# Kernel tuning notes

Measured on AMD Instinct MI355X. Metric: run time of the kernel, lower is better.

## Reference

```python
import jax, jax.numpy as jnp
import numpy as np

N_NODES = 100000
N_EDGES = 1200000
NUM_GRAPHS = 128
IN_DIM = 5
HIDDEN = 64


def setup_inputs() -> dict:
    key = jax.random.key(0)
    ks = jax.random.split(key, 12)
    x = jax.random.normal(ks[0], (N_NODES, IN_DIM), dtype=jnp.float32)
    edge_index = jax.random.randint(ks[1], (2, N_EDGES), 0, N_NODES, dtype=jnp.int64 if jax.config.read('jax_enable_x64') else jnp.int32)
    batch = jnp.sort(jax.random.randint(ks[2], (N_NODES,), 0, NUM_GRAPHS, dtype=jnp.int32))
    s = lambda fan_in: 1.0 / np.sqrt(fan_in)
    return {
        'x': x,
        'edge_index': edge_index,
        'batch': batch,
        'w_rel1': jax.random.normal(ks[3], (IN_DIM, HIDDEN), dtype=jnp.float32) * s(IN_DIM),
        'b_rel1': jnp.zeros((HIDDEN,), dtype=jnp.float32),
        'w_root1': jax.random.normal(ks[4], (IN_DIM, HIDDEN), dtype=jnp.float32) * s(IN_DIM),
        'w_rel2': jax.random.normal(ks[5], (HIDDEN, HIDDEN), dtype=jnp.float32) * s(HIDDEN),
        'b_rel2': jnp.zeros((HIDDEN,), dtype=jnp.float32),
        'w_root2': jax.random.normal(ks[6], (HIDDEN, HIDDEN), dtype=jnp.float32) * s(HIDDEN),
        'w_h1': jax.random.normal(ks[7], (2 * HIDDEN, HIDDEN), dtype=jnp.float32) * s(2 * HIDDEN),
        'b_h1': jnp.zeros((HIDDEN,), dtype=jnp.float32),
        'w_h2': jax.random.normal(ks[8], (HIDDEN, 1), dtype=jnp.float32) * s(HIDDEN),
        'b_h2': jnp.zeros((1,), dtype=jnp.float32),
    }


def _graph_conv(x, src, dst, w_rel, b_rel, w_root):
    # PyG GraphConv (aggr='add'): out = aggr(x_src -> dst) @ W_rel + b_rel + x @ W_root
    agg = jax.ops.segment_sum(x[src], dst, num_segments=N_NODES)
    return agg @ w_rel + b_rel + x @ w_root


def reference(x, edge_index, batch,
              w_rel1, b_rel1, w_root1,
              w_rel2, b_rel2, w_root2,
              w_h1, b_h1, w_h2, b_h2):
    src, dst = edge_index[0], edge_index[1]
    h = jax.nn.relu(_graph_conv(x, src, dst, w_rel1, b_rel1, w_root1))
    h = jax.nn.relu(_graph_conv(h, src, dst, w_rel2, b_rel2, w_root2))
    # global add + mean pooling over graphs
    add_pool = jax.ops.segment_sum(h, batch, num_segments=NUM_GRAPHS)
    counts = jax.ops.segment_sum(jnp.ones((N_NODES,), h.dtype), batch, num_segments=NUM_GRAPHS)
    mean_pool = add_pool / jnp.maximum(counts, 1.0)[:, None]
    g = jnp.concatenate([mean_pool, add_pool], axis=1)  # [G, 2*HIDDEN]
    out = jax.nn.relu(g @ w_h1 + b_h1) @ w_h2 + b_h2
    return out.squeeze(-1)
```

## Files before the change

kernel.cpp:

```cpp
#include <hip/hip_runtime.h>
#include <hip/hip_bf16.h>

#define N_NODES    100000
#define N_EDGES    1200000
#define NUM_GRAPHS 128
#define IN_DIM     5
#define HIDDEN     64
#define M_TILES    (N_NODES / 16)
#define NI4        (N_EDGES / 4)

#define CB    391
#define CBLK  256
#define EPB   ((NI4 + CBLK - 1) / CBLK)

typedef __attribute__((ext_vector_type(8))) short short8;
typedef __attribute__((ext_vector_type(4))) float f32x4;

__device__ __forceinline__ unsigned short f2bs(float f) {
    union { float f; unsigned u; } v; v.f = f;
    return (unsigned short)((v.u + 0x7FFFu + ((v.u >> 16) & 1u)) >> 16);
}
__device__ __forceinline__ float bs2f(unsigned short s) {
    union { unsigned u; float f; } v; v.u = ((unsigned)s) << 16;
    return v.f;
}
__device__ __forceinline__ float blo(unsigned p) { return bs2f((unsigned short)(p & 0xffff)); }
__device__ __forceinline__ float bhi(unsigned p) { return bs2f((unsigned short)(p >> 16)); }
__device__ __forceinline__ unsigned pack2(float a, float b) {
    return ((unsigned)f2bs(b) << 16) | (unsigned)f2bs(a);
}

__device__ __forceinline__ unsigned char f2f8(float f) {
    union { float f; unsigned u; } v; v.f = f * 0x1p-120f;
    unsigned u = v.u + 0x7FFFFu + ((v.u >> 20) & 1u);
    return (unsigned char)(u >> 20);
}
__device__ __forceinline__ float f82f(unsigned b) {
    union { unsigned u; float f; } v; v.u = (b & 0x7Fu) << 20;
    return v.f * 0x1p120f;
}


__global__ void coarse_count(const int* __restrict__ dst, int* __restrict__ gcnt,
                             const float* __restrict__ x, uint4* __restrict__ xb) {
    __shared__ int h[CB];
    int t = threadIdx.x, b = blockIdx.x;
    for (int i = t; i < CB; i += 256) h[i] = 0;
    __syncthreads();
    int i0 = b * EPB, i1 = min(i0 + EPB, NI4);
    for (int i = i0 + t; i < i1; i += 256) {
        int4 d = ((const int4*)dst)[i];
        atomicAdd(&h[d.x >> 8], 1);
        atomicAdd(&h[d.y >> 8], 1);
        atomicAdd(&h[d.z >> 8], 1);
        atomicAdd(&h[d.w >> 8], 1);
    }
    __syncthreads();
    for (int i = t; i < CB; i += 256) gcnt[b * CB + i] = h[i];

    for (int n = b * 256 + t; n < N_NODES; n += CBLK * 256) {
        const float* xr = x + (size_t)n * IN_DIM;
        uint4 o;
        o.x = pack2(xr[0], xr[1]);
        o.y = pack2(xr[2], xr[3]);
        o.z = pack2(xr[4], 0.0f);
        o.w = 0u;
        xb[n] = o;
    }
}

__global__ void block_scan(int* __restrict__ gcnt, int* __restrict__ btot) {
    __shared__ int s[CBLK];
    int k = blockIdx.x, t = threadIdx.x;
    int v = gcnt[t * CB + k];
    s[t] = v;
    __syncthreads();
    for (int off = 1; off < CBLK; off <<= 1) {
        int u = (t >= off) ? s[t - off] : 0;
        __syncthreads();
        s[t] += u;
        __syncthreads();
    }
    gcnt[t * CB + k] = s[t] - v;
    if (t == CBLK - 1) btot[k] = s[t];
}

__global__ void bucket_scan(const int* __restrict__ btot, int* __restrict__ bstart,
                            float* __restrict__ add_pool, int* __restrict__ ptr) {
    __shared__ int s[512];
    int t = threadIdx.x;
    int v = (t < CB) ? btot[t] : 0;
    s[t] = v;
    __syncthreads();
    for (int off = 1; off < 512; off <<= 1) {
        int u = (t >= off) ? s[t - off] : 0;
        __syncthreads();
        s[t] += u;
        __syncthreads();
    }
    if (t < CB) bstart[t] = s[t] - v;
    if (t == 0) { bstart[CB] = N_EDGES; ptr[N_NODES] = N_EDGES; }
    for (int i = t; i < NUM_GRAPHS * HIDDEN; i += 512) add_pool[i] = 0.0f;
}

__global__ void partition_k(const int* __restrict__ src, const int* __restrict__ dst,
                            const int* __restrict__ gcnt, const int* __restrict__ bstart,
                            int* __restrict__ part) {
    __shared__ int base[CB];
    __shared__ int h[CB];
    int t = threadIdx.x, b = blockIdx.x;
    for (int i = t; i < CB; i += 256) {
        base[i] = bstart[i] + gcnt[b * CB + i];
        h[i] = 0;
    }
    __syncthreads();
    int i0 = b * EPB, i1 = min(i0 + EPB, NI4);
    for (int i = i0 + t; i < i1; i += 256) {
        int4 s4 = ((const int4*)src)[i];
        int4 d4 = ((const int4*)dst)[i];
        int k, r;
        k = d4.x >> 8; r = atomicAdd(&h[k], 1); part[base[k] + r] = s4.x | ((d4.x & 255) << 17);
        k = d4.y >> 8; r = atomicAdd(&h[k], 1); part[base[k] + r] = s4.y | ((d4.y & 255) << 17);
        k = d4.z >> 8; r = atomicAdd(&h[k], 1); part[base[k] + r] = s4.z | ((d4.z & 255) << 17);
        k = d4.w >> 8; r = atomicAdd(&h[k], 1); part[base[k] + r] = s4.w | ((d4.w & 255) << 17);
    }
}

__global__ void fine_sort(const int* __restrict__ part, const int* __restrict__ bstart,
                          int* __restrict__ ptr, int* __restrict__ esrc) {
    __shared__ int fh[256];
    __shared__ int fo[256];
    __shared__ int fr[256];
    int k = blockIdx.x, t = threadIdx.x;
    int e0 = bstart[k], e1 = bstart[k + 1];
    fh[t] = 0; fr[t] = 0;
    __syncthreads();
    for (int e = e0 + t; e < e1; e += 256)
        atomicAdd(&fh[(part[e] >> 17) & 255], 1);
    __syncthreads();
    int v = fh[t];
    fo[t] = v;
    __syncthreads();
    for (int off = 1; off < 256; off <<= 1) {
        int u = (t >= off) ? fo[t - off] : 0;
        __syncthreads();
        fo[t] += u;
        __syncthreads();
    }
    int excl = fo[t] - v;
    int n = (k << 8) + t;
    if (n < N_NODES) ptr[n] = e0 + excl;
    fh[t] = excl;
    __syncthreads();
    for (int e = e0 + t; e < e1; e += 256) {
        int p = part[e];
        int d = (p >> 17) & 255;
        int r = atomicAdd(&fr[d], 1);
        esrc[e0 + fh[d] + r] = p & 0x1FFFF;
    }
}


__global__ void gather_mlp1(const uint4* __restrict__ xb,
                            const float* __restrict__ x,
                            const int* __restrict__ ptr,
                            const int* __restrict__ esrc,
                            const float* __restrict__ w_rel1,
                            const float* __restrict__ b_rel1,
                            const float* __restrict__ w_root1,
                            unsigned short* __restrict__ h1,
                            unsigned char* __restrict__ h1f8) {
    int t    = threadIdx.x;
    int ql   = t & 15;
    int grp  = (blockIdx.x * blockDim.x + t) >> 4;
    int ngrp = (gridDim.x * blockDim.x) >> 4;

    float wr[IN_DIM][4], wo[IN_DIM][4], bias[4];
#pragma unroll
    for (int j = 0; j < 4; ++j) {
        int ch = ql * 4 + j;
        bias[j] = b_rel1[ch];
#pragma unroll
        for (int k = 0; k < IN_DIM; ++k) {
            wr[k][j] = w_rel1[k * HIDDEN + ch];
            wo[k][j] = w_root1[k * HIDDEN + ch];
        }
    }

    for (int n = grp; n < N_NODES; n += ngrp) {
        int start = ptr[n], end = ptr[n + 1];
        float a[IN_DIM] = {0.f, 0.f, 0.f, 0.f, 0.f};
        for (int e = start + ql; e < end; e += 16) {
            uint4 p = xb[esrc[e]];
            a[0] += blo(p.x); a[1] += bhi(p.x);
            a[2] += blo(p.y); a[3] += bhi(p.y);
            a[4] += blo(p.z);
        }
#pragma unroll
        for (int k = 0; k < IN_DIM; ++k) {
            a[k] += __shfl_xor(a[k], 1, 64);
            a[k] += __shfl_xor(a[k], 2, 64);
            a[k] += __shfl_xor(a[k], 4, 64);
            a[k] += __shfl_xor(a[k], 8, 64);
        }
        float xr[IN_DIM];
#pragma unroll
        for (int k = 0; k < IN_DIM; ++k) xr[k] = x[(size_t)n * IN_DIM + k];

        unsigned short hv[4];
        unsigned char  hf[4];
#pragma unroll
        for (int j = 0; j < 4; ++j) {
            float acc = bias[j];
#pragma unroll
            for (int k = 0; k < IN_DIM; ++k)
                acc += a[k] * wr[k][j] + xr[k] * wo[k][j];
            float h = fmaxf(acc, 0.0f);
            hv[j] = f2bs(h);
            hf[j] = f2f8(h);
        }
        ushort4 v4; v4.x = hv[0]; v4.y = hv[1]; v4.z = hv[2]; v4.w = hv[3];
        *(ushort4*)(h1 + (size_t)n * HIDDEN + ql * 4) = v4;
        uchar4 c4; c4.x = hf[0]; c4.y = hf[1]; c4.z = hf[2]; c4.w = hf[3];
        *(uchar4*)(h1f8 + (size_t)n * HIDDEN + ql * 4) = c4;
    }
}

__global__ void gather2_fp8(const unsigned* __restrict__ rows,
                            const int* __restrict__ ptr,
                            const int* __restrict__ esrc,
                            uint2* __restrict__ agg2) {
    int t    = threadIdx.x;
    int ql   = t & 15;
    int grp  = (blockIdx.x * blockDim.x + t) >> 4;
    int ngrp = (gridDim.x * blockDim.x) >> 4;

    for (int n = grp; n < N_NODES; n += ngrp) {
        int start = ptr[n], end = ptr[n + 1];
        float4 a = {0.f, 0.f, 0.f, 0.f};
        float4 b = {0.f, 0.f, 0.f, 0.f};
        int e = start;
        for (; e + 1 < end; e += 2) {
            int s0 = esrc[e], s1 = esrc[e + 1];
            unsigned r0 = rows[(size_t)s0 * 16 + ql];
            unsigned r1 = rows[(size_t)s1 * 16 + ql];
            a.x += f82f(r0); a.y += f82f(r0 >> 8); a.z += f82f(r0 >> 16); a.w += f82f(r0 >> 24);
            b.x += f82f(r1); b.y += f82f(r1 >> 8); b.z += f82f(r1 >> 16); b.w += f82f(r1 >> 24);
        }
        if (e < end) {
            unsigned r0 = rows[(size_t)esrc[e] * 16 + ql];
            a.x += f82f(r0); a.y += f82f(r0 >> 8); a.z += f82f(r0 >> 16); a.w += f82f(r0 >> 24);
        }
        a.x += b.x; a.y += b.y; a.z += b.z; a.w += b.w;
        uint2 o;
        o.x = pack2(a.x, a.y);
        o.y = pack2(a.z, a.w);
        agg2[(size_t)n * 16 + ql] = o;
    }
}

__global__ void mlp2_pool(const unsigned short* __restrict__ agg2,
                          const unsigned short* __restrict__ h1,
                          const float* __restrict__ w_rel2,
                          const float* __restrict__ b_rel2,
                          const float* __restrict__ w_root2,
                          const int* __restrict__ batch,
                          float* __restrict__ add_pool) {
    int lane = threadIdx.x & 63;
    int wv   = threadIdx.x >> 6;
    int row  = lane & 15;
    int quad = lane >> 4;
    int n    = wv * 16 + row;

    short8 bwr[2], bwo[2];
#pragma unroll
    for (int s = 0; s < 2; ++s)
#pragma unroll
        for (int j = 0; j < 8; ++j) {
            int k = 32 * s + quad * 8 + j;
            bwr[s][j] = (short)f2bs(w_rel2[k * HIDDEN + n]);
            bwo[s][j] = (short)f2bs(w_root2[k * HIDDEN + n]);
        }
    float bias = b_rel2[n];

    for (int t = blockIdx.x; t < M_TILES; t += gridDim.x) {
        int m0 = t * 16;
        size_t rbase = (size_t)(m0 + row) * HIDDEN;
        short8 aa0 = *(const short8*)(agg2 + rbase + quad * 8);
        short8 aa1 = *(const short8*)(agg2 + rbase + 32 + quad * 8);
        short8 ah0 = *(const short8*)(h1   + rbase + quad * 8);
        short8 ah1 = *(const short8*)(h1   + rbase + 32 + quad * 8);

        f32x4 acc = {bias, bias, bias, bias};
        acc = __builtin_amdgcn_mfma_f32_16x16x32_bf16(aa0, bwr[0], acc, 0, 0, 0);
        acc = __builtin_amdgcn_mfma_f32_16x16x32_bf16(aa1, bwr[1], acc, 0, 0, 0);
        acc = __builtin_amdgcn_mfma_f32_16x16x32_bf16(ah0, bwo[0], acc, 0, 0, 0);
        acc = __builtin_amdgcn_mfma_f32_16x16x32_bf16(ah1, bwo[1], acc, 0, 0, 0);

        float hv0 = fmaxf(acc[0], 0.0f), hv1 = fmaxf(acc[1], 0.0f);
        float hv2 = fmaxf(acc[2], 0.0f), hv3 = fmaxf(acc[3], 0.0f);

        int gLo = batch[m0], gHi = batch[m0 + 15];
        if (gLo == gHi) {
            float s = (hv0 + hv1) + (hv2 + hv3);
            s += __shfl_xor(s, 16, 64);
            s += __shfl_xor(s, 32, 64);
            if (quad == 0)
                atomicAdd(&add_pool[gLo * HIDDEN + n], s);
        } else {
            int m = m0 + quad * 4;
            atomicAdd(&add_pool[batch[m]     * HIDDEN + n], hv0);
            atomicAdd(&add_pool[batch[m + 1] * HIDDEN + n], hv1);
            atomicAdd(&add_pool[batch[m + 2] * HIDDEN + n], hv2);
            atomicAdd(&add_pool[batch[m + 3] * HIDDEN + n], hv3);
        }
    }
}

__device__ __forceinline__ int lower_bound_i(const int* a, int n, int v) {
    int lo = 0, hi = n;
    while (lo < hi) { int mid = (lo + hi) >> 1; if (a[mid] < v) lo = mid + 1; else hi = mid; }
    return lo;
}

__global__ void head_mlp(const float* __restrict__ add_pool,
                         const int* __restrict__ batch,
                         const float* __restrict__ w_h1,
                         const float* __restrict__ b_h1,
                         const float* __restrict__ w_h2,
                         const float* __restrict__ b_h2,
                         float* __restrict__ out) {
    int g = blockIdx.x, t = threadIdx.x;

    __shared__ int s_cnt;
    if (t == 0) {
        int start = lower_bound_i(batch, N_NODES, g);
        int end   = lower_bound_i(batch, N_NODES, g + 1);
        s_cnt = end - start;
    }
    __syncthreads();
    float cnt = fmaxf((float)s_cnt, 1.0f);

    __shared__ float sg[2 * HIDDEN];
    float add = add_pool[(size_t)g * HIDDEN + t];
    sg[t]          = add / cnt;
    sg[HIDDEN + t] = add;
    __syncthreads();

    float hid = b_h1[t];
#pragma unroll 16
    for (int i = 0; i < 2 * HIDDEN; ++i)
        hid += sg[i] * w_h1[i * HIDDEN + t];
    hid = fmaxf(hid, 0.0f);

    float res = hid * w_h2[t];
    for (int off = 32; off > 0; off >>= 1)
        res += __shfl_down(res, off, 64);
    if (t == 0) out[g] = res + b_h2[0];
}

extern "C" void kernel_launch(void* const* d_in, const int* in_sizes, int n_in,
                              void* d_out, int out_size, void* d_ws, size_t ws_size,
                              hipStream_t stream) {
    const float* x       = (const float*)d_in[0];
    const int*   ei      = (const int*)d_in[1];
    const int*   src     = ei;
    const int*   dst     = ei + N_EDGES;
    const int*   batch   = (const int*)d_in[2];
    const float* w_rel1  = (const float*)d_in[3];
    const float* b_rel1  = (const float*)d_in[4];
    const float* w_root1 = (const float*)d_in[5];
    const float* w_rel2  = (const float*)d_in[6];
    const float* b_rel2  = (const float*)d_in[7];
    const float* w_root2 = (const float*)d_in[8];
    const float* w_h1    = (const float*)d_in[9];
    const float* b_h1    = (const float*)d_in[10];
    const float* w_h2    = (const float*)d_in[11];
    const float* b_h2    = (const float*)d_in[12];
    float* out = (float*)d_out;

    int* base = (int*)d_ws;
    int*   gcnt     = base;
    int*   btot     = gcnt + ((CBLK * CB + 3) & ~3);
    int*   bstart   = btot + ((CB + 3) & ~3);
    float* add_pool = (float*)(bstart + ((CB + 1 + 3) & ~3));
    int*   ptr      = (int*)(add_pool + NUM_GRAPHS * HIDDEN);
    int*   part     = ptr + ((N_NODES + 1 + 3) & ~3);
    int*   esrc     = part + N_EDGES;
    unsigned short* h1   = (unsigned short*)(esrc + N_EDGES);
    unsigned short* agg2 = h1 + (size_t)N_NODES * HIDDEN;
    unsigned char*  h1f8 = (unsigned char*)(agg2 + (size_t)N_NODES * HIDDEN);
    uint4*          xb   = (uint4*)(h1f8 + (size_t)N_NODES * HIDDEN);

    coarse_count<<<CBLK, 256, 0, stream>>>(dst, gcnt, x, xb);
    block_scan<<<CB, CBLK, 0, stream>>>(gcnt, btot);
    bucket_scan<<<1, 512, 0, stream>>>(btot, bstart, add_pool, ptr);
    partition_k<<<CBLK, 256, 0, stream>>>(src, dst, gcnt, bstart, part);
    fine_sort<<<CB, 256, 0, stream>>>(part, bstart, ptr, esrc);

    gather_mlp1<<<2048, 256, 0, stream>>>(xb, x, ptr, esrc, w_rel1, b_rel1, w_root1, h1, h1f8);
    gather2_fp8<<<2048, 256, 0, stream>>>((const unsigned*)h1f8, ptr, esrc, (uint2*)agg2);
    mlp2_pool<<<2048, 256, 0, stream>>>(agg2, h1, w_rel2, b_rel2, w_root2, batch, add_pool);
    head_mlp<<<NUM_GRAPHS, 64, 0, stream>>>(add_pool, batch, w_h1, b_h1, w_h2, b_h2, out);
}
```

Measured before the change: 191.2 us.

## Fuse fine sort with first-layer gather and unroll fp8 gather by four

The per-bucket fine sort kernel now goes on to compute layer-1 aggregation and the MLP for its 256 nodes, using the shared-memory offsets instead of re-reading ptr. This removes a kernel launch and lets the esrc entries just written be reused from cache. The cost is that the 391 blocks of this stage now carry the gather work, with less parallelism than the separate 2048-block launch. Separately, the second-layer fp8 gather is unrolled to four independent accumulators to raise memory-level parallelism.

New measurement: 195.4 us. 1.02x slower.

```diff
diff --git a/kernel.cpp b/kernel.cpp
--- a/kernel.cpp
+++ b/kernel.cpp
@@ -126,8 +126,15 @@
     }
 }
 
-__global__ void fine_sort(const int* __restrict__ part, const int* __restrict__ bstart,
-                          int* __restrict__ ptr, int* __restrict__ esrc) {
+__global__ void fine_gather1(const int* __restrict__ part, const int* __restrict__ bstart,
+                             int* __restrict__ ptr, int* __restrict__ esrc,
+                             const uint4* __restrict__ xb,
+                             const float* __restrict__ x,
+                             const float* __restrict__ w_rel1,
+                             const float* __restrict__ b_rel1,
+                             const float* __restrict__ w_root1,
+                             unsigned short* __restrict__ h1,
+                             unsigned char* __restrict__ h1f8) {
     __shared__ int fh[256];
     __shared__ int fo[256];
     __shared__ int fr[256];
@@ -148,8 +155,8 @@
         __syncthreads();
     }
     int excl = fo[t] - v;
-    int n = (k << 8) + t;
-    if (n < N_NODES) ptr[n] = e0 + excl;
+    int n_t = (k << 8) + t;
+    if (n_t < N_NODES) ptr[n_t] = e0 + excl;
     fh[t] = excl;
     __syncthreads();
     for (int e = e0 + t; e < e1; e += 256) {
@@ -158,37 +165,27 @@
         int r = atomicAdd(&fr[d], 1);
         esrc[e0 + fh[d] + r] = p & 0x1FFFF;
     }
-}
-
-
-__global__ void gather_mlp1(const uint4* __restrict__ xb,
-                            const float* __restrict__ x,
-                            const int* __restrict__ ptr,
-                            const int* __restrict__ esrc,
-                            const float* __restrict__ w_rel1,
-                            const float* __restrict__ b_rel1,
-                            const float* __restrict__ w_root1,
-                            unsigned short* __restrict__ h1,
-                            unsigned char* __restrict__ h1f8) {
-    int t    = threadIdx.x;
-    int ql   = t & 15;
-    int grp  = (blockIdx.x * blockDim.x + t) >> 4;
-    int ngrp = (gridDim.x * blockDim.x) >> 4;
-
+    __syncthreads();
+
+    int ql = t & 15;
+    int g  = t >> 4;
     float wr[IN_DIM][4], wo[IN_DIM][4], bias[4];
 #pragma unroll
     for (int j = 0; j < 4; ++j) {
         int ch = ql * 4 + j;
         bias[j] = b_rel1[ch];
 #pragma unroll
-        for (int k = 0; k < IN_DIM; ++k) {
-            wr[k][j] = w_rel1[k * HIDDEN + ch];
-            wo[k][j] = w_root1[k * HIDDEN + ch];
-        }
-    }
-
-    for (int n = grp; n < N_NODES; n += ngrp) {
-        int start = ptr[n], end = ptr[n + 1];
+        for (int kk = 0; kk < IN_DIM; ++kk) {
+            wr[kk][j] = w_rel1[kk * HIDDEN + ch];
+            wo[kk][j] = w_root1[kk * HIDDEN + ch];
+        }
+    }
+
+    for (int nl = g; nl < 256; nl += 16) {
+        int n = (k << 8) + nl;
+        if (n >= N_NODES) break;
+        int start = e0 + fh[nl];
+        int end   = (nl < 255) ? (e0 + fh[nl + 1]) : e1;
         float a[IN_DIM] = {0.f, 0.f, 0.f, 0.f, 0.f};
         for (int e = start + ql; e < end; e += 16) {
             uint4 p = xb[esrc[e]];
@@ -197,15 +194,15 @@
             a[4] += blo(p.z);
         }
 #pragma unroll
-        for (int k = 0; k < IN_DIM; ++k) {
-            a[k] += __shfl_xor(a[k], 1, 64);
-            a[k] += __shfl_xor(a[k], 2, 64);
-            a[k] += __shfl_xor(a[k], 4, 64);
-            a[k] += __shfl_xor(a[k], 8, 64);
+        for (int kk = 0; kk < IN_DIM; ++kk) {
+            a[kk] += __shfl_xor(a[kk], 1, 64);
+            a[kk] += __shfl_xor(a[kk], 2, 64);
+            a[kk] += __shfl_xor(a[kk], 4, 64);
+            a[kk] += __shfl_xor(a[kk], 8, 64);
         }
         float xr[IN_DIM];
 #pragma unroll
-        for (int k = 0; k < IN_DIM; ++k) xr[k] = x[(size_t)n * IN_DIM + k];
+        for (int kk = 0; kk < IN_DIM; ++kk) xr[kk] = x[(size_t)n * IN_DIM + kk];
 
         unsigned short hv[4];
         unsigned char  hf[4];
@@ -213,8 +210,8 @@
         for (int j = 0; j < 4; ++j) {
             float acc = bias[j];
 #pragma unroll
-            for (int k = 0; k < IN_DIM; ++k)
-                acc += a[k] * wr[k][j] + xr[k] * wo[k][j];
+            for (int kk = 0; kk < IN_DIM; ++kk)
+                acc += a[kk] * wr[kk][j] + xr[kk] * wo[kk][j];
             float h = fmaxf(acc, 0.0f);
             hv[j] = f2bs(h);
             hf[j] = f2f8(h);
@@ -225,6 +222,7 @@
         *(uchar4*)(h1f8 + (size_t)n * HIDDEN + ql * 4) = c4;
     }
 }
+
 
 __global__ void gather2_fp8(const unsigned* __restrict__ rows,
                             const int* __restrict__ ptr,
@@ -237,21 +235,28 @@
 
     for (int n = grp; n < N_NODES; n += ngrp) {
         int start = ptr[n], end = ptr[n + 1];
-        float4 a = {0.f, 0.f, 0.f, 0.f};
-        float4 b = {0.f, 0.f, 0.f, 0.f};
+        float4 a0 = {0.f,0.f,0.f,0.f}, a1 = a0, a2 = a0, a3 = a0;
         int e = start;
-        for (; e + 1 < end; e += 2) {
-            int s0 = esrc[e], s1 = esrc[e + 1];
+        for (; e + 3 < end; e += 4) {
+            int s0 = esrc[e], s1 = esrc[e + 1], s2 = esrc[e + 2], s3 = esrc[e + 3];
             unsigned r0 = rows[(size_t)s0 * 16 + ql];
             unsigned r1 = rows[(size_t)s1 * 16 + ql];
-            a.x += f82f(r0); a.y += f82f(r0 >> 8); a.z += f82f(r0 >> 16); a.w += f82f(r0 >> 24);
-            b.x += f82f(r1); b.y += f82f(r1 >> 8); b.z += f82f(r1 >> 16); b.w += f82f(r1 >> 24);
-        }
-        if (e < end) {
+            unsigned r2 = rows[(size_t)s2 * 16 + ql];
+            unsigned r3 = rows[(size_t)s3 * 16 + ql];
+            a0.x += f82f(r0); a0.y += f82f(r0 >> 8); a0.z += f82f(r0 >> 16); a0.w += f82f(r0 >> 24);
+            a1.x += f82f(r1); a1.y += f82f(r1 >> 8); a1.z += f82f(r1 >> 16); a1.w += f82f(r1 >> 24);
+            a2.x += f82f(r2); a2.y += f82f(r2 >> 8); a2.z += f82f(r2 >> 16); a2.w += f82f(r2 >> 24);
+            a3.x += f82f(r3); a3.y += f82f(r3 >> 8); a3.z += f82f(r3 >> 16); a3.w += f82f(r3 >> 24);
+        }
+        for (; e < end; ++e) {
             unsigned r0 = rows[(size_t)esrc[e] * 16 + ql];
-            a.x += f82f(r0); a.y += f82f(r0 >> 8); a.z += f82f(r0 >> 16); a.w += f82f(r0 >> 24);
-        }
-        a.x += b.x; a.y += b.y; a.z += b.z; a.w += b.w;
+            a0.x += f82f(r0); a0.y += f82f(r0 >> 8); a0.z += f82f(r0 >> 16); a0.w += f82f(r0 >> 24);
+        }
+        float4 a;
+        a.x = (a0.x + a1.x) + (a2.x + a3.x);
+        a.y = (a0.y + a1.y) + (a2.y + a3.y);
+        a.z = (a0.z + a1.z) + (a2.z + a3.z);
+        a.w = (a0.w + a1.w) + (a2.w + a3.w);
         uint2 o;
         o.x = pack2(a.x, a.y);
         o.y = pack2(a.z, a.w);
@@ -396,9 +401,9 @@
     block_scan<<<CB, CBLK, 0, stream>>>(gcnt, btot);
     bucket_scan<<<1, 512, 0, stream>>>(btot, bstart, add_pool, ptr);
     partition_k<<<CBLK, 256, 0, stream>>>(src, dst, gcnt, bstart, part);
-    fine_sort<<<CB, 256, 0, stream>>>(part, bstart, ptr, esrc);
-
-    gather_mlp1<<<2048, 256, 0, stream>>>(xb, x, ptr, esrc, w_rel1, b_rel1, w_root1, h1, h1f8);
+
+    fine_gather1<<<CB, 256, 0, stream>>>(part, bstart, ptr, esrc, xb, x,
+                                         w_rel1, b_rel1, w_root1, h1, h1f8);
     gather2_fp8<<<2048, 256, 0, stream>>>((const unsigned*)h1f8, ptr, esrc, (uint2*)agg2);
     mlp2_pool<<<2048, 256, 0, stream>>>(agg2, h1, w_rel2, b_rel2, w_root2, batch, add_pool);
     head_mlp<<<NUM_GRAPHS, 64, 0, stream>>>(add_pool, batch, w_h1, b_h1, w_h2, b_h2, out);
```
